# Performance work log

Hardware: AMD Instinct MI355X
Metric: run time of the kernel (lower is better)

The kernel has to match this reference:

```python
import jax, jax.numpy as jnp
import numpy as np

N_TOKEN = 50000
D_EMBED = 512
D_PROJ = 1024
CUTOFFS = [10000, 30000, 50000]  # cutoffs + [n_token]
N_CLUSTERS = len(CUTOFFS) - 1    # 2


def setup_inputs() -> dict:
    key = jax.random.key(0)
    ks = jax.random.split(key, 8)
    s = 0.02
    return {
        "hidden": jax.random.normal(ks[0], (4096, D_PROJ), jnp.float32),
        "target": jax.random.randint(ks[1], (4096,), 0, N_TOKEN, jnp.int64),
        # div_val == 1: one big output embedding, sliced per cluster
        "weight": jax.random.normal(ks[2], (N_TOKEN, D_EMBED), jnp.float32) * s,
        "bias": jnp.zeros((N_TOKEN,), jnp.float32),
        "cluster_weight": jax.random.normal(ks[3], (N_CLUSTERS, D_EMBED), jnp.float32) * s,
        "cluster_bias": jnp.zeros((N_CLUSTERS,), jnp.float32),
        # one [d_proj, d_embed] projection per cluster (head + 2 tails)
        "projs": jax.random.normal(ks[4], (N_CLUSTERS + 1, D_PROJ, D_EMBED), jnp.float32) * s,
    }


def _adaptive_logprob(hidden, target, weight, bias, cluster_weight, cluster_bias, projs):
    c0 = CUTOFFS[0]
    n = hidden.shape[0]
    # head: first-cluster vocab + one logit per tail cluster
    head_w = jnp.concatenate([weight[:c0], cluster_weight], axis=0)      # [c0+K, d_embed]
    head_b = jnp.concatenate([bias[:c0], cluster_bias], axis=0)          # [c0+K]
    h0 = hidden @ projs[0]                                               # [N, d_embed]
    head_lp = jax.nn.log_softmax(h0 @ head_w.T + head_b, axis=-1)        # [N, c0+K]

    # tokens in head cluster
    head_idx = jnp.clip(target, 0, c0 - 1)
    lp = jnp.take_along_axis(head_lp, head_idx[:, None], axis=1)[:, 0]
    out = jnp.where(target < c0, lp, 0.0)

    # tail clusters
    for i in range(1, N_CLUSTERS + 1):
        l, r = CUTOFFS[i - 1], CUTOFFS[i]
        hi = hidden @ projs[i]                                           # [N, d_embed]
        tail_lp = jax.nn.log_softmax(hi @ weight[l:r].T + bias[l:r], axis=-1)  # [N, r-l]
        t_idx = jnp.clip(target - l, 0, r - l - 1)
        tlp = jnp.take_along_axis(tail_lp, t_idx[:, None], axis=1)[:, 0]
        lp_i = head_lp[:, c0 + i - 1] + tlp
        out = jnp.where((target >= l) & (target < r), lp_i, out)

    return -out  # nll per token, [N]


def reference(hidden, target, weight, bias, cluster_weight, cluster_bias, projs):
    tgt_len = target.shape[0]
    nll = _adaptive_logprob(hidden[-tgt_len:], target, weight, bias,
                            cluster_weight, cluster_bias, projs)
    return nll.reshape(tgt_len, -1)  # [N, 1], matches loss.view(tgt_len, -1)
```

## Files before the change

kernel.cpp:

```cpp
#include <hip/hip_runtime.h>
#include <math.h>

#define NT 4096
#define DP 1024
#define DE 512
#define C0 10000
#define CUT1 30000
#define TAILV 20000
#define WROWS 50240
#define NBH 40
#define NBT 79

typedef unsigned short ushort_t;
typedef short bf8 __attribute__((ext_vector_type(8)));
typedef float f4 __attribute__((ext_vector_type(4)));

__device__ __forceinline__ ushort_t f2b(float f) {
    union { float f; unsigned int u; } v; v.f = f;
    unsigned int r = v.u + 0x7FFFu + ((v.u >> 16) & 1u);
    return (ushort_t)(r >> 16);
}
__device__ __forceinline__ float b2f(ushort_t u) {
    union { unsigned int u; float f; } v; v.u = ((unsigned int)u) << 16; return v.f;
}

__device__ __forceinline__ void gld16(const void* g, void* l) {
    __builtin_amdgcn_global_load_lds(
        (const __attribute__((address_space(1))) unsigned int*)g,
        (__attribute__((address_space(3))) unsigned int*)l, 16, 0, 0);
}

__device__ __forceinline__ int xcd_swz(int wgid, int nwg) {
    int q = nwg >> 3, r = nwg & 7;
    int xcd = wgid & 7, idx = wgid >> 3;
    int base = (xcd < r) ? xcd * (q + 1) : r * (q + 1) + (xcd - r) * q;
    return base + idx;
}

__global__ void cluster_kernel(const int* __restrict__ target,
                               int* __restrict__ cnt, int* __restrict__ list) {
    int t = blockIdx.x * blockDim.x + threadIdx.x;
    if (t >= NT) return;
    int tgt = target[t];
    int c = (tgt < C0) ? 0 : (tgt < CUT1 ? 1 : 2);
    if (c > 0) {
        int pos = atomicAdd(&cnt[c - 1], 1);
        list[(c - 1) * NT + pos] = t;
    }
}

__global__ __launch_bounds__(256)
void cast_pad(const float* __restrict__ in, ushort_t* __restrict__ out,
              int total4, int valid) {
    int i = blockIdx.x * 256 + threadIdx.x;
    if (i >= total4) return;
    int base = i * 4;
    unsigned long long p = 0ull;
    if (base < valid) {
        float4 v = *reinterpret_cast<const float4*>(in + base);
        p = (unsigned long long)f2b(v.x)
          | ((unsigned long long)f2b(v.y) << 16)
          | ((unsigned long long)f2b(v.z) << 32)
          | ((unsigned long long)f2b(v.w) << 48);
    }
    *reinterpret_cast<unsigned long long*>(out + base) = p;
}

__global__ __launch_bounds__(256)
void transpose_cast(const float* __restrict__ projs, ushort_t* __restrict__ out) {
    const int cblk = blockIdx.z;
    const int n0 = blockIdx.x * 32;
    const int k0 = blockIdx.y * 32;
    __shared__ float tile[32][33];
    const int tx = threadIdx.x & 31, ty = threadIdx.x >> 5;
    const float* src = projs + (size_t)cblk * DP * DE;
    #pragma unroll
    for (int j = 0; j < 4; ++j)
        tile[ty + j * 8][tx] = src[(size_t)(k0 + ty + j * 8) * DE + n0 + tx];
    __syncthreads();
    ushort_t* dst = out + (size_t)cblk * DE * DP;
    #pragma unroll
    for (int j = 0; j < 4; ++j)
        dst[(size_t)(n0 + ty + j * 8) * DP + k0 + tx] = f2b(tile[tx][ty + j * 8]);
}

template<int MODE>
__global__ __launch_bounds__(512, 2)
void gemm_bt(const ushort_t* __restrict__ Ab, const ushort_t* __restrict__ Bb,
             ushort_t* __restrict__ Cout, float* __restrict__ Sout,
             const float* __restrict__ bias,
             const int* __restrict__ cnt, const int* __restrict__ list,
             int K, int validN)
{
    const int tid = threadIdx.x;
    const int lane = tid & 63;
    const int w = tid >> 6;
    const int wm = w >> 2, wn = w & 3;

    const int logical = xcd_swz(blockIdx.x, gridDim.x);
    const int bm = (logical & 15) * 256;
    const int bn = (logical >> 4) * 256;
    const int nb = logical >> 4;

    int n = 0;
    if (MODE == 0) {
        Bb += (size_t)blockIdx.z * DE * DP;
        Cout += (size_t)blockIdx.z * (size_t)NT * DE;
    }
    if (MODE == 2) {
        const int tail = blockIdx.z;
        n = cnt[tail];
        if (bm >= n) return;
        Ab += (size_t)(1 + tail) * NT * DE;
        Bb += (size_t)(C0 + tail * TAILV) * DE;
        bias += C0 + tail * TAILV;
        list += tail * NT;
        Sout += (size_t)tail * NBT * NT;
    }

    __shared__ __align__(16) unsigned char lds[131072];

    const int kswz = (lane & 7) ^ (lane >> 3);
    const int dstoff = (w * 8 + (lane >> 3)) * 128 + (lane & 7) * 16;

    const char* ap[4];
    const char* bp[4];
    #pragma unroll
    for (int i = 0; i < 4; ++i) {
        int r = i * 64 + w * 8 + (lane >> 3);
        int ga;
        if (MODE == 2) {
            int gr = bm + r;
            ga = (gr < n) ? list[gr] : 0;
        } else ga = bm + r;
        ap[i] = (const char*)Ab + (size_t)ga * K * 2 + kswz * 16;
        bp[i] = (const char*)Bb + (size_t)(bn + r) * K * 2 + kswz * 16;
    }

    f4 acc[8][4];
    const f4 zero = {0.f, 0.f, 0.f, 0.f};
    #pragma unroll
    for (int i = 0; i < 8; ++i)
        #pragma unroll
        for (int j = 0; j < 4; ++j) acc[i][j] = zero;

    auto stage = [&](int t, unsigned char* buf) {
        const int kb = t << 7;
        #pragma unroll
        for (int i = 0; i < 4; ++i) {
            gld16(ap[i] + kb, buf + i * 8192 + dstoff);
            gld16(bp[i] + kb, buf + 32768 + i * 8192 + dstoff);
        }
    };

    const int ntiles = K >> 6;
    stage(0, lds);
    __syncthreads();

    for (int t = 0; t < ntiles; ++t) {
        unsigned char* cur = lds + ((t & 1) ? 65536 : 0);
        if (t + 1 < ntiles)
            stage(t + 1, lds + (((t + 1) & 1) ? 65536 : 0));
        const unsigned char* As = cur;
        const unsigned char* Bs = cur + 32768;
        #pragma unroll
        for (int kh = 0; kh < 2; ++kh) {
            bf8 bv[4];
            #pragma unroll
            for (int nf = 0; nf < 4; ++nf) {
                const int Rb = wn * 64 + nf * 16 + (lane & 15);
                bv[nf] = *reinterpret_cast<const bf8*>(
                    Bs + Rb * 128 + (((kh * 4 + (lane >> 4)) ^ (Rb & 7)) << 4));
            }
            #pragma unroll
            for (int mf = 0; mf < 8; ++mf) {
                const int Ra = wm * 128 + mf * 16 + (lane & 15);
                bf8 af = *reinterpret_cast<const bf8*>(
                    As + Ra * 128 + (((kh * 4 + (lane >> 4)) ^ (Ra & 7)) << 4));
                #pragma unroll
                for (int nf = 0; nf < 4; ++nf)
                    acc[mf][nf] = __builtin_amdgcn_mfma_f32_16x16x32_bf16(
                        af, bv[nf], acc[mf][nf], 0, 0, 0);
            }
        }
        __syncthreads();
    }

    if (MODE == 0) {
        #pragma unroll
        for (int mf = 0; mf < 8; ++mf) {
            const int row = bm + wm * 128 + mf * 16 + ((lane >> 4) << 2);
            #pragma unroll
            for (int nf = 0; nf < 4; ++nf) {
                const int col = bn + wn * 64 + nf * 16 + (lane & 15);
                #pragma unroll
                for (int r = 0; r < 4; ++r)
                    Cout[(size_t)(row + r) * DE + col] = f2b(acc[mf][nf][r]);
            }
        }
    } else {
        float rs[8][4];
        #pragma unroll
        for (int mf = 0; mf < 8; ++mf)
            #pragma unroll
            for (int r = 0; r < 4; ++r) {
                float s = 0.f;
                #pragma unroll
                for (int nf = 0; nf < 4; ++nf) {
                    const int col = bn + wn * 64 + nf * 16 + (lane & 15);
                    if (col < validN) s += __expf(acc[mf][nf][r] + bias[col]);
                }
                rs[mf][r] = s;
            }
        #pragma unroll
        for (int m = 1; m < 16; m <<= 1)
            #pragma unroll
            for (int mf = 0; mf < 8; ++mf)
                #pragma unroll
                for (int r = 0; r < 4; ++r)
                    rs[mf][r] += __shfl_xor(rs[mf][r], m);
        float* ps = (float*)lds;
        if ((lane & 15) == 0) {
            const int rb = (lane >> 4) << 2;
            #pragma unroll
            for (int mf = 0; mf < 8; ++mf)
                #pragma unroll
                for (int r = 0; r < 4; ++r)
                    ps[wn * 256 + wm * 128 + mf * 16 + rb + r] = rs[mf][r];
        }
        __syncthreads();
        if (tid < 256) {
            float v = ps[tid] + ps[256 + tid] + ps[512 + tid] + ps[768 + tid];
            Sout[(size_t)nb * NT + bm + tid] = v;
        }
    }
}

__global__ __launch_bounds__(256)
void reduce_kernel(const float* __restrict__ Ph, const float* __restrict__ Pt,
                   const int* __restrict__ cnt, const int* __restrict__ list,
                   float* __restrict__ S_head, float* __restrict__ S_tail) {
    const int z = blockIdx.y;
    const int t = blockIdx.x * 256 + threadIdx.x;
    if (z == 0) {
        if (t >= NT) return;
        float s = 0.f;
        for (int nb = 0; nb < NBH; ++nb) s += Ph[(size_t)nb * NT + t];
        S_head[t] = s;
    } else {
        const int tail = z - 1;
        if (t >= cnt[tail]) return;
        const float* P = Pt + (size_t)tail * NBT * NT;
        float s = 0.f;
        for (int nb = 0; nb < NBT; ++nb) s += P[(size_t)nb * NT + t];
        S_tail[list[tail * NT + t]] = s;
    }
}

__global__ __launch_bounds__(64)
void finalize_kernel(const ushort_t* __restrict__ Hb, const int* __restrict__ target,
                     const float* __restrict__ weight, const float* __restrict__ bias,
                     const float* __restrict__ cw, const float* __restrict__ cb,
                     const float* __restrict__ S_head, const float* __restrict__ S_tail,
                     float* __restrict__ out)
{
    const int t = blockIdx.x, lane = threadIdx.x;
    const int tgt = target[t];
    const int c = (tgt < C0) ? 0 : (tgt < CUT1 ? 1 : 2);
    const int e = lane * 8;

    union { uint4 u; ushort_t s[8]; } h0;
    h0.u = *reinterpret_cast<const uint4*>(Hb + (size_t)t * DE + e);
    float hv[8];
    #pragma unroll
    for (int k = 0; k < 8; ++k) hv[k] = b2f(h0.s[k]);

    float c1 = 0.f, c2 = 0.f;
    #pragma unroll
    for (int k = 0; k < 8; ++k) {
        c1 += hv[k] * cw[e + k];
        c2 += hv[k] * cw[DE + e + k];
    }

    const ushort_t* hs = (c == 0) ? (Hb + (size_t)t * DE)
                                  : (Hb + ((size_t)c * NT + (size_t)t) * DE);
    union { uint4 u; ushort_t s[8]; } hc;
    hc.u = *reinterpret_cast<const uint4*>(hs + e);
    const float* wt = weight + (size_t)tgt * DE;
    float dt = 0.f;
    #pragma unroll
    for (int k = 0; k < 8; ++k) dt += b2f(hc.s[k]) * wt[e + k];

    #pragma unroll
    for (int m = 32; m; m >>= 1) {
        c1 += __shfl_xor(c1, m);
        c2 += __shfl_xor(c2, m);
        dt += __shfl_xor(dt, m);
    }
    if (lane == 0) {
        c1 += cb[0]; c2 += cb[1];
        const float S = S_head[t] + __expf(c1) + __expf(c2);
        const float lsh = logf(S);
        float res;
        if (c == 0) {
            res = lsh - (dt + bias[tgt]);
        } else {
            const float cl = (c == 1) ? c1 : c2;
            res = (lsh - cl) + (logf(S_tail[t]) - (dt + bias[tgt]));
        }
        out[t] = res;
    }
}

extern "C" void kernel_launch(void* const* d_in, const int* in_sizes, int n_in,
                              void* d_out, int out_size, void* d_ws, size_t ws_size,
                              hipStream_t stream) {
    const float* hidden = (const float*)d_in[0];
    const int*   target = (const int*)d_in[1];
    const float* weight = (const float*)d_in[2];
    const float* bias   = (const float*)d_in[3];
    const float* cw     = (const float*)d_in[4];
    const float* cb     = (const float*)d_in[5];
    const float* projs  = (const float*)d_in[6];
    float* out = (float*)d_out;

    char* w = (char*)d_ws;
    ushort_t* Hb      = (ushort_t*)w;  w += (size_t)3 * NT * DE * 2;
    ushort_t* hiddenb = (ushort_t*)w;  w += (size_t)NT * DP * 2;
    ushort_t* Wb      = (ushort_t*)w;  w += (size_t)WROWS * DE * 2;
    ushort_t* projsTb = (ushort_t*)w;  w += (size_t)3 * DE * DP * 2;
    float* S_head = (float*)w;         w += NT * 4;
    float* S_tail = (float*)w;         w += NT * 4;
    int* cnt      = (int*)w;           w += 32;
    int* list     = (int*)w;           w += 2 * NT * 4;
    float* Ph     = (float*)w;         w += (size_t)NBH * NT * 4;
    float* Pt     = (float*)w;         w += (size_t)2 * NBT * NT * 4;

    hipMemsetAsync(cnt, 0, 32, stream);
    cluster_kernel<<<NT / 256, 256, 0, stream>>>(target, cnt, list);
    cast_pad<<<(NT * DP / 4 + 255) / 256, 256, 0, stream>>>(
        hidden, hiddenb, NT * DP / 4, NT * DP);
    cast_pad<<<(WROWS * DE / 4 + 255) / 256, 256, 0, stream>>>(
        weight, Wb, WROWS * DE / 4, 50000 * DE);
    transpose_cast<<<dim3(DE / 32, DP / 32, 3), 256, 0, stream>>>(projs, projsTb);

    gemm_bt<0><<<dim3(16 * 2, 1, 3), 512, 0, stream>>>(
        hiddenb, projsTb, Hb, nullptr, nullptr, nullptr, nullptr, DP, DE);
    gemm_bt<1><<<dim3(16 * NBH, 1, 1), 512, 0, stream>>>(
        Hb, Wb, nullptr, Ph, bias, nullptr, nullptr, DE, C0);
    gemm_bt<2><<<dim3(16 * NBT, 1, 2), 512, 0, stream>>>(
        Hb, Wb, nullptr, Pt, bias, cnt, list, DE, TAILV);
    reduce_kernel<<<dim3(NT / 256, 3), 256, 0, stream>>>(
        Ph, Pt, cnt, list, S_head, S_tail);
    finalize_kernel<<<NT, 64, 0, stream>>>(
        Hb, target, weight, bias, cw, cb, S_head, S_tail, out);
}
```

Before: 319.7 us.

## Template GEMM tiles, prefetch two stages ahead with vmcnt waits, smaller projection tiles

After: 320.6 us. Within noise of the previous version (+0.3%).

```diff
diff --git a/kernel.cpp b/kernel.cpp
--- a/kernel.cpp
+++ b/kernel.cpp
@@ -28,6 +28,13 @@
     __builtin_amdgcn_global_load_lds(
         (const __attribute__((address_space(1))) unsigned int*)g,
         (__attribute__((address_space(3))) unsigned int*)l, 16, 0, 0);
+}
+
+template<int N> __device__ __forceinline__ void waitcnt_vm() {
+    if constexpr (N == 0)      asm volatile("s_waitcnt vmcnt(0)" ::: "memory");
+    else if constexpr (N == 4) asm volatile("s_waitcnt vmcnt(4)" ::: "memory");
+    else if constexpr (N == 8) asm volatile("s_waitcnt vmcnt(8)" ::: "memory");
+    else if constexpr (N == 12) asm volatile("s_waitcnt vmcnt(12)" ::: "memory");
 }
 
 __device__ __forceinline__ int xcd_swz(int wgid, int nwg) {
@@ -84,23 +91,33 @@
         dst[(size_t)(n0 + ty + j * 8) * DP + k0 + tx] = f2b(tile[tx][ty + j * 8]);
 }
 
-template<int MODE>
-__global__ __launch_bounds__(512, 2)
+template<int MODE, int BM, int BN, int KK, int MINW>
+__global__ __launch_bounds__(512, MINW)
 void gemm_bt(const ushort_t* __restrict__ Ab, const ushort_t* __restrict__ Bb,
              ushort_t* __restrict__ Cout, float* __restrict__ Sout,
              const float* __restrict__ bias,
              const int* __restrict__ cnt, const int* __restrict__ list,
-             int K, int validN)
+             int validN)
 {
+    constexpr int NTILES = KK >> 6;
+    constexpr int NLA = BM / 64;
+    constexpr int NLB = BN / 64;
+    constexpr int S = NLA + NLB;
+    constexpr int MF = BM / 32;
+    constexpr int NF = BN / 64;
+    constexpr int MBLK = NT / BM;
+    constexpr int ABYTES = BM * 128;
+    constexpr int BUF = (BM + BN) * 128;
+
     const int tid = threadIdx.x;
     const int lane = tid & 63;
     const int w = tid >> 6;
     const int wm = w >> 2, wn = w & 3;
 
     const int logical = xcd_swz(blockIdx.x, gridDim.x);
-    const int bm = (logical & 15) * 256;
-    const int bn = (logical >> 4) * 256;
-    const int nb = logical >> 4;
+    const int bm = (logical % MBLK) * BM;
+    const int bn = (logical / MBLK) * BN;
+    const int nb = logical / MBLK;
 
     int n = 0;
     if (MODE == 0) {
@@ -118,96 +135,107 @@
         Sout += (size_t)tail * NBT * NT;
     }
 
-    __shared__ __align__(16) unsigned char lds[131072];
+    __shared__ __align__(16) unsigned char lds[2 * BUF];
 
     const int kswz = (lane & 7) ^ (lane >> 3);
     const int dstoff = (w * 8 + (lane >> 3)) * 128 + (lane & 7) * 16;
 
-    const char* ap[4];
-    const char* bp[4];
-    #pragma unroll
-    for (int i = 0; i < 4; ++i) {
+    const char* ap[NLA];
+    const char* bp[NLB];
+    #pragma unroll
+    for (int i = 0; i < NLA; ++i) {
         int r = i * 64 + w * 8 + (lane >> 3);
         int ga;
         if (MODE == 2) {
             int gr = bm + r;
             ga = (gr < n) ? list[gr] : 0;
         } else ga = bm + r;
-        ap[i] = (const char*)Ab + (size_t)ga * K * 2 + kswz * 16;
-        bp[i] = (const char*)Bb + (size_t)(bn + r) * K * 2 + kswz * 16;
-    }
-
-    f4 acc[8][4];
+        ap[i] = (const char*)Ab + (size_t)ga * KK * 2 + kswz * 16;
+    }
+    #pragma unroll
+    for (int i = 0; i < NLB; ++i) {
+        int r = i * 64 + w * 8 + (lane >> 3);
+        bp[i] = (const char*)Bb + (size_t)(bn + r) * KK * 2 + kswz * 16;
+    }
+
+    f4 acc[MF][NF];
     const f4 zero = {0.f, 0.f, 0.f, 0.f};
     #pragma unroll
-    for (int i = 0; i < 8; ++i)
-        #pragma unroll
-        for (int j = 0; j < 4; ++j) acc[i][j] = zero;
+    for (int i = 0; i < MF; ++i)
+        #pragma unroll
+        for (int j = 0; j < NF; ++j) acc[i][j] = zero;
 
     auto stage = [&](int t, unsigned char* buf) {
         const int kb = t << 7;
         #pragma unroll
-        for (int i = 0; i < 4; ++i) {
+        for (int i = 0; i < NLA; ++i)
             gld16(ap[i] + kb, buf + i * 8192 + dstoff);
-            gld16(bp[i] + kb, buf + 32768 + i * 8192 + dstoff);
-        }
+        #pragma unroll
+        for (int i = 0; i < NLB; ++i)
+            gld16(bp[i] + kb, buf + ABYTES + i * 8192 + dstoff);
     };
 
-    const int ntiles = K >> 6;
     stage(0, lds);
-    __syncthreads();
-
-    for (int t = 0; t < ntiles; ++t) {
-        unsigned char* cur = lds + ((t & 1) ? 65536 : 0);
-        if (t + 1 < ntiles)
-            stage(t + 1, lds + (((t + 1) & 1) ? 65536 : 0));
-        const unsigned char* As = cur;
-        const unsigned char* Bs = cur + 32768;
+    stage(1, lds + BUF);
+
+    #pragma unroll
+    for (int t = 0; t < NTILES; ++t) {
+        if (t == NTILES - 1) waitcnt_vm<0>();
+        else                 waitcnt_vm<S>();
+        __builtin_amdgcn_s_barrier();
+        __builtin_amdgcn_sched_barrier(0);
+        const unsigned char* As = lds + (t & 1) * BUF;
+        const unsigned char* Bs = As + ABYTES;
+        __builtin_amdgcn_s_setprio(1);
         #pragma unroll
         for (int kh = 0; kh < 2; ++kh) {
-            bf8 bv[4];
-            #pragma unroll
-            for (int nf = 0; nf < 4; ++nf) {
-                const int Rb = wn * 64 + nf * 16 + (lane & 15);
+            bf8 bv[NF];
+            #pragma unroll
+            for (int nf = 0; nf < NF; ++nf) {
+                const int Rb = wn * (BN / 4) + nf * 16 + (lane & 15);
                 bv[nf] = *reinterpret_cast<const bf8*>(
                     Bs + Rb * 128 + (((kh * 4 + (lane >> 4)) ^ (Rb & 7)) << 4));
             }
             #pragma unroll
-            for (int mf = 0; mf < 8; ++mf) {
-                const int Ra = wm * 128 + mf * 16 + (lane & 15);
+            for (int mf = 0; mf < MF; ++mf) {
+                const int Ra = wm * (BM / 2) + mf * 16 + (lane & 15);
                 bf8 af = *reinterpret_cast<const bf8*>(
                     As + Ra * 128 + (((kh * 4 + (lane >> 4)) ^ (Ra & 7)) << 4));
                 #pragma unroll
-                for (int nf = 0; nf < 4; ++nf)
+                for (int nf = 0; nf < NF; ++nf)
                     acc[mf][nf] = __builtin_amdgcn_mfma_f32_16x16x32_bf16(
                         af, bv[nf], acc[mf][nf], 0, 0, 0);
             }
         }
-        __syncthreads();
+        __builtin_amdgcn_s_setprio(0);
+        __builtin_amdgcn_sched_barrier(0);
+        asm volatile("s_waitcnt lgkmcnt(0)" ::: "memory");
+        __builtin_amdgcn_s_barrier();
+        if (t + 2 < NTILES) stage(t + 2, lds + (t & 1) * BUF);
     }
 
     if (MODE == 0) {
         #pragma unroll
-        for (int mf = 0; mf < 8; ++mf) {
-            const int row = bm + wm * 128 + mf * 16 + ((lane >> 4) << 2);
-            #pragma unroll
-            for (int nf = 0; nf < 4; ++nf) {
-                const int col = bn + wn * 64 + nf * 16 + (lane & 15);
+        for (int mf = 0; mf < MF; ++mf) {
+            const int row = bm + wm * (BM / 2) + mf * 16 + ((lane >> 4) << 2);
+            #pragma unroll
+            for (int nf = 0; nf < NF; ++nf) {
+                const int col = bn + wn * (BN / 4) + nf * 16 + (lane & 15);
                 #pragma unroll
                 for (int r = 0; r < 4; ++r)
                     Cout[(size_t)(row + r) * DE + col] = f2b(acc[mf][nf][r]);
             }
         }
     } else {
-        float rs[8][4];
-        #pragma unroll
-        for (int mf = 0; mf < 8; ++mf)
+        float rs[MF][4];
+        #pragma unroll
+        for (int mf = 0; mf < MF; ++mf)
             #pragma unroll
             for (int r = 0; r < 4; ++r) {
                 float s = 0.f;
                 #pragma unroll
-                for (int nf = 0; nf < 4; ++nf) {
-                    const int col = bn + wn * 64 + nf * 16 + (lane & 15);
+                for (int nf = 0; nf < NF; ++nf) {
+                    const int col = bn + wn * (BN / 4) + nf * 16 + (lane & 15);
                     if (col < validN) s += __expf(acc[mf][nf][r] + bias[col]);
                 }
                 rs[mf][r] = s;
@@ -215,7 +243,7 @@
         #pragma unroll
         for (int m = 1; m < 16; m <<= 1)
             #pragma unroll
-            for (int mf = 0; mf < 8; ++mf)
+            for (int mf = 0; mf < MF; ++mf)
                 #pragma unroll
                 for (int r = 0; r < 4; ++r)
                     rs[mf][r] += __shfl_xor(rs[mf][r], m);
@@ -223,14 +251,14 @@
         if ((lane & 15) == 0) {
             const int rb = (lane >> 4) << 2;
             #pragma unroll
-            for (int mf = 0; mf < 8; ++mf)
+            for (int mf = 0; mf < MF; ++mf)
                 #pragma unroll
                 for (int r = 0; r < 4; ++r)
-                    ps[wn * 256 + wm * 128 + mf * 16 + rb + r] = rs[mf][r];
+                    ps[wn * BM + wm * (BM / 2) + mf * 16 + rb + r] = rs[mf][r];
         }
         __syncthreads();
-        if (tid < 256) {
-            float v = ps[tid] + ps[256 + tid] + ps[512 + tid] + ps[768 + tid];
+        if (tid < BM) {
+            float v = ps[tid] + ps[BM + tid] + ps[2 * BM + tid] + ps[3 * BM + tid];
             Sout[(size_t)nb * NT + bm + tid] = v;
         }
     }
@@ -344,12 +372,12 @@
         weight, Wb, WROWS * DE / 4, 50000 * DE);
     transpose_cast<<<dim3(DE / 32, DP / 32, 3), 256, 0, stream>>>(projs, projsTb);
 
-    gemm_bt<0><<<dim3(16 * 2, 1, 3), 512, 0, stream>>>(
-        hiddenb, projsTb, Hb, nullptr, nullptr, nullptr, nullptr, DP, DE);
-    gemm_bt<1><<<dim3(16 * NBH, 1, 1), 512, 0, stream>>>(
-        Hb, Wb, nullptr, Ph, bias, nullptr, nullptr, DE, C0);
-    gemm_bt<2><<<dim3(16 * NBT, 1, 2), 512, 0, stream>>>(
-        Hb, Wb, nullptr, Pt, bias, cnt, list, DE, TAILV);
+    gemm_bt<0, 128, 128, 1024, 4><<<dim3(32 * 4, 1, 3), 512, 0, stream>>>(
+        hiddenb, projsTb, Hb, nullptr, nullptr, nullptr, nullptr, DE);
+    gemm_bt<1, 256, 256, 512, 2><<<dim3(16 * NBH, 1, 1), 512, 0, stream>>>(
+        Hb, Wb, nullptr, Ph, bias, nullptr, nullptr, C0);
+    gemm_bt<2, 256, 256, 512, 2><<<dim3(16 * NBT, 1, 2), 512, 0, stream>>>(
+        Hb, Wb, nullptr, Pt, bias, cnt, list, TAILV);
     reduce_kernel<<<dim3(NT / 256, 3), 256, 0, stream>>>(
         Ph, Pt, cnt, list, S_head, S_tail);
     finalize_kernel<<<NT, 64, 0, stream>>>(
```

## Merge head and tail logit GEMMs and software-pipeline the MFMA main loop

Applied to the files above, without the earlier changes.

Result: slower. 409.9 us (+28.2%).

```diff
diff --git a/kernel.cpp b/kernel.cpp
--- a/kernel.cpp
+++ b/kernel.cpp
@@ -84,58 +84,84 @@
         dst[(size_t)(n0 + ty + j * 8) * DP + k0 + tx] = f2b(tile[tx][ty + j * 8]);
 }
 
-template<int MODE>
+template<int MODE, int KK>
 __global__ __launch_bounds__(512, 2)
-void gemm_bt(const ushort_t* __restrict__ Ab, const ushort_t* __restrict__ Bb,
-             ushort_t* __restrict__ Cout, float* __restrict__ Sout,
-             const float* __restrict__ bias,
-             const int* __restrict__ cnt, const int* __restrict__ list,
-             int K, int validN)
+void gemm8(const ushort_t* __restrict__ A0, const ushort_t* __restrict__ B0,
+           ushort_t* __restrict__ Cout, float* __restrict__ Ph,
+           float* __restrict__ Pt, const float* __restrict__ bias,
+           const int* __restrict__ cnt, const int* __restrict__ list)
 {
+    constexpr int NTL = KK >> 6;
     const int tid = threadIdx.x;
     const int lane = tid & 63;
     const int w = tid >> 6;
     const int wm = w >> 2, wn = w & 3;
 
     const int logical = xcd_swz(blockIdx.x, gridDim.x);
-    const int bm = (logical & 15) * 256;
-    const int bn = (logical >> 4) * 256;
-    const int nb = logical >> 4;
-
-    int n = 0;
+    int mb, nb, validN = 0, n = 0, seg = 0;
+    const ushort_t* Ab;
+    const ushort_t* Bb;
+    float* Sout = nullptr;
+    const float* bvec = nullptr;
+
     if (MODE == 0) {
-        Bb += (size_t)blockIdx.z * DE * DP;
+        mb = logical & 15; nb = logical >> 4;
+        Ab = A0;
+        Bb = B0 + (size_t)blockIdx.z * DE * DP;
         Cout += (size_t)blockIdx.z * (size_t)NT * DE;
-    }
-    if (MODE == 2) {
-        const int tail = blockIdx.z;
-        n = cnt[tail];
-        if (bm >= n) return;
-        Ab += (size_t)(1 + tail) * NT * DE;
-        Bb += (size_t)(C0 + tail * TAILV) * DE;
-        bias += C0 + tail * TAILV;
-        list += tail * NT;
-        Sout += (size_t)tail * NBT * NT;
-    }
+    } else {
+        int l = logical;
+        if (l < 16 * NBH) { seg = 0; }
+        else if (l < 16 * (NBH + NBT)) { seg = 1; l -= 16 * NBH; }
+        else { seg = 2; l -= 16 * (NBH + NBT); }
+        mb = l & 15; nb = l >> 4;
+        if (seg == 0) {
+            Ab = A0; Bb = B0; bvec = bias; validN = C0; Sout = Ph;
+        } else {
+            const int z = seg - 1;
+            n = cnt[z];
+            if (mb * 256 >= n) return;
+            Ab = A0 + (size_t)(1 + z) * NT * DE;
+            Bb = B0 + (size_t)(C0 + z * TAILV) * DE;
+            bvec = bias + C0 + z * TAILV;
+            list += z * NT;
+            validN = TAILV;
+            Sout = Pt + (size_t)z * NBT * NT;
+        }
+    }
+    const int bm = mb * 256, bn = nb * 256;
 
     __shared__ __align__(16) unsigned char lds[131072];
 
-    const int kswz = (lane & 7) ^ (lane >> 3);
-    const int dstoff = (w * 8 + (lane >> 3)) * 128 + (lane & 7) * 16;
+    const int kswz = (tid & 7) ^ ((tid >> 3) & 7);
+    const int dstoff = (tid >> 3) * 128 + (tid & 7) * 16;
 
     const char* ap[4];
     const char* bp[4];
     #pragma unroll
     for (int i = 0; i < 4; ++i) {
-        int r = i * 64 + w * 8 + (lane >> 3);
-        int ga;
-        if (MODE == 2) {
+        int r = i * 64 + (tid >> 3);
+        int ga = bm + r;
+        if (MODE == 1 && seg > 0) {
             int gr = bm + r;
-            ga = (gr < n) ? list[gr] : 0;
-        } else ga = bm + r;
-        ap[i] = (const char*)Ab + (size_t)ga * K * 2 + kswz * 16;
-        bp[i] = (const char*)Bb + (size_t)(bn + r) * K * 2 + kswz * 16;
-    }
+            ga = list[(gr < n) ? gr : 0];
+        }
+        ap[i] = (const char*)Ab + (size_t)ga * KK * 2 + kswz * 16;
+        bp[i] = (const char*)Bb + (size_t)(bn + r) * KK * 2 + kswz * 16;
+    }
+
+    auto stageA = [&](int h, int t, int b) {
+        unsigned char* base = lds + b * 65536 + h * 16384 + dstoff;
+        const int kb = t << 7;
+        gld16(ap[2 * h] + kb, base);
+        gld16(ap[2 * h + 1] + kb, base + 8192);
+    };
+    auto stageB = [&](int h, int t, int b) {
+        unsigned char* base = lds + b * 65536 + 32768 + h * 16384 + dstoff;
+        const int kb = t << 7;
+        gld16(bp[2 * h] + kb, base);
+        gld16(bp[2 * h + 1] + kb, base + 8192);
+    };
 
     f4 acc[8][4];
     const f4 zero = {0.f, 0.f, 0.f, 0.f};
@@ -144,47 +170,87 @@
         #pragma unroll
         for (int j = 0; j < 4; ++j) acc[i][j] = zero;
 
-    auto stage = [&](int t, unsigned char* buf) {
-        const int kb = t << 7;
-        #pragma unroll
-        for (int i = 0; i < 4; ++i) {
-            gld16(ap[i] + kb, buf + i * 8192 + dstoff);
-            gld16(bp[i] + kb, buf + 32768 + i * 8192 + dstoff);
-        }
+    bf8 afr[4][2], bv01[2][2], bv23[2][2];
+
+    auto rdAf = [&](int mfb, const unsigned char* Abase) {
+        #pragma unroll
+        for (int m = 0; m < 4; ++m)
+            #pragma unroll
+            for (int kh = 0; kh < 2; ++kh) {
+                const int Ra = wm * 128 + (mfb + m) * 16 + (lane & 15);
+                afr[m][kh] = *reinterpret_cast<const bf8*>(
+                    Abase + Ra * 128 + (((kh * 4 + (lane >> 4)) ^ (Ra & 7)) << 4));
+            }
     };
-
-    const int ntiles = K >> 6;
-    stage(0, lds);
-    __syncthreads();
-
-    for (int t = 0; t < ntiles; ++t) {
-        unsigned char* cur = lds + ((t & 1) ? 65536 : 0);
-        if (t + 1 < ntiles)
-            stage(t + 1, lds + (((t + 1) & 1) ? 65536 : 0));
-        const unsigned char* As = cur;
-        const unsigned char* Bs = cur + 32768;
-        #pragma unroll
-        for (int kh = 0; kh < 2; ++kh) {
-            bf8 bv[4];
-            #pragma unroll
-            for (int nf = 0; nf < 4; ++nf) {
-                const int Rb = wn * 64 + nf * 16 + (lane & 15);
-                bv[nf] = *reinterpret_cast<const bf8*>(
-                    Bs + Rb * 128 + (((kh * 4 + (lane >> 4)) ^ (Rb & 7)) << 4));
+    auto rdBv = [&](bf8 (&bv)[2][2], int nfb, const unsigned char* Bbase) {
+        #pragma unroll
+        for (int j = 0; j < 2; ++j)
+            #pragma unroll
+            for (int kh = 0; kh < 2; ++kh) {
+                const int Rb = wn * 64 + (nfb + j) * 16 + (lane & 15);
+                bv[j][kh] = *reinterpret_cast<const bf8*>(
+                    Bbase + Rb * 128 + (((kh * 4 + (lane >> 4)) ^ (Rb & 7)) << 4));
             }
-            #pragma unroll
-            for (int mf = 0; mf < 8; ++mf) {
-                const int Ra = wm * 128 + mf * 16 + (lane & 15);
-                bf8 af = *reinterpret_cast<const bf8*>(
-                    As + Ra * 128 + (((kh * 4 + (lane >> 4)) ^ (Ra & 7)) << 4));
-                #pragma unroll
-                for (int nf = 0; nf < 4; ++nf)
-                    acc[mf][nf] = __builtin_amdgcn_mfma_f32_16x16x32_bf16(
-                        af, bv[nf], acc[mf][nf], 0, 0, 0);
-            }
-        }
-        __syncthreads();
-    }
+    };
+
+#define CLUSTER(MB, JB, BV)                                                  \
+    do {                                                                     \
+        __builtin_amdgcn_s_setprio(1);                                       \
+        _Pragma("unroll")                                                    \
+        for (int kh = 0; kh < 2; ++kh)                                       \
+            _Pragma("unroll")                                                \
+            for (int m = 0; m < 4; ++m)                                      \
+                _Pragma("unroll")                                            \
+                for (int j = 0; j < 2; ++j)                                  \
+                    acc[MB + m][JB + j] =                                    \
+                        __builtin_amdgcn_mfma_f32_16x16x32_bf16(             \
+                            afr[m][kh], BV[j][kh], acc[MB + m][JB + j],      \
+                            0, 0, 0);                                        \
+        __builtin_amdgcn_s_setprio(0);                                       \
+    } while (0)
+
+    stageB(0, 0, 0); stageB(1, 0, 0);
+    stageA(0, 0, 0); stageA(1, 0, 0);
+    stageB(0, 1, 1); stageB(1, 1, 1);
+
+    for (int g = 0; g < NTL; ++g) {
+        const int b = g & 1;
+        const unsigned char* Abase = lds + b * 65536;
+        const unsigned char* Bbase = Abase + 32768;
+
+        if (g == NTL - 1) asm volatile("s_waitcnt vmcnt(0)" ::: "memory");
+        else              asm volatile("s_waitcnt vmcnt(4)" ::: "memory");
+        __builtin_amdgcn_s_barrier();
+        __builtin_amdgcn_sched_barrier(0);
+        rdAf(0, Abase);
+        rdBv(bv01, 0, Bbase);
+        asm volatile("s_waitcnt lgkmcnt(0)" ::: "memory");
+        __builtin_amdgcn_sched_barrier(0);
+        CLUSTER(0, 0, bv01);
+        if (g + 1 < NTL) stageA(0, g + 1, b ^ 1);
+
+        __builtin_amdgcn_s_barrier();
+        __builtin_amdgcn_sched_barrier(0);
+        rdBv(bv23, 2, Bbase);
+        asm volatile("s_waitcnt lgkmcnt(0)" ::: "memory");
+        __builtin_amdgcn_sched_barrier(0);
+        CLUSTER(0, 2, bv23);
+        if (g + 1 < NTL) stageA(1, g + 1, b ^ 1);
+
+        __builtin_amdgcn_s_barrier();
+        __builtin_amdgcn_sched_barrier(0);
+        rdAf(4, Abase);
+        asm volatile("s_waitcnt lgkmcnt(0)" ::: "memory");
+        __builtin_amdgcn_sched_barrier(0);
+        CLUSTER(4, 2, bv23);
+        if (g + 2 < NTL) stageB(0, g + 2, b);
+
+        __builtin_amdgcn_s_barrier();
+        __builtin_amdgcn_sched_barrier(0);
+        CLUSTER(4, 0, bv01);
+        if (g + 2 < NTL) stageB(1, g + 2, b);
+    }
+#undef CLUSTER
 
     if (MODE == 0) {
         #pragma unroll
@@ -208,7 +274,7 @@
                 #pragma unroll
                 for (int nf = 0; nf < 4; ++nf) {
                     const int col = bn + wn * 64 + nf * 16 + (lane & 15);
-                    if (col < validN) s += __expf(acc[mf][nf][r] + bias[col]);
+                    if (col < validN) s += __expf(acc[mf][nf][r] + bvec[col]);
                 }
                 rs[mf][r] = s;
             }
@@ -219,6 +285,7 @@
                 #pragma unroll
                 for (int r = 0; r < 4; ++r)
                     rs[mf][r] += __shfl_xor(rs[mf][r], m);
+        __syncthreads();
         float* ps = (float*)lds;
         if ((lane & 15) == 0) {
             const int rb = (lane >> 4) << 2;
@@ -344,12 +411,11 @@
         weight, Wb, WROWS * DE / 4, 50000 * DE);
     transpose_cast<<<dim3(DE / 32, DP / 32, 3), 256, 0, stream>>>(projs, projsTb);
 
-    gemm_bt<0><<<dim3(16 * 2, 1, 3), 512, 0, stream>>>(
-        hiddenb, projsTb, Hb, nullptr, nullptr, nullptr, nullptr, DP, DE);
-    gemm_bt<1><<<dim3(16 * NBH, 1, 1), 512, 0, stream>>>(
-        Hb, Wb, nullptr, Ph, bias, nullptr, nullptr, DE, C0);
-    gemm_bt<2><<<dim3(16 * NBT, 1, 2), 512, 0, stream>>>(
-        Hb, Wb, nullptr, Pt, bias, cnt, list, DE, TAILV);
+    gemm8<0, DP><<<dim3(32, 1, 3), 512, 0, stream>>>(
+        hiddenb, projsTb, Hb, nullptr, nullptr, nullptr, nullptr, nullptr);
+    gemm8<1, DE><<<dim3(16 * (NBH + 2 * NBT), 1, 1), 512, 0, stream>>>(
+        Hb, Wb, nullptr, Ph, Pt, bias, cnt, list);
+
     reduce_kernel<<<dim3(NT / 256, 3), 256, 0, stream>>>(
         Ph, Pt, cnt, list, S_head, S_tail);
     finalize_kernel<<<NT, 64, 0, stream>>>(
```
